# Optimization experiments

Measured on AMD Instinct MI355X. Metric: run time of the kernel, lower is better.

The kernel has to match this reference:

```python
import jax, jax.numpy as jnp
import numpy as np

H, W = 256, 256
S, S_IDX, END_BIAS = 48, 3, 10
E_IDX = S - END_BIAS          # 38
N_ITER = E_IDX - (S_IDX + 1)  # 34 sequential segments after the start segment
OUT_WIN = 10                  # outlier1d window length
OUT_THRESH = 2.0


def setup_inputs() -> dict:
    key = jax.random.key(0)
    # (x, y) event coordinates in [0, W) x [0, H); t/p/b columns are unused by the module.
    events = jax.random.uniform(key, (16, 960000, 2), jnp.float32, minval=0.0, maxval=256.0)
    return {"events": events}


def _blur(a):
    """5x5 uniform (0.04) blur, SAME padding; a: [B, S, D] -> [B, S, D]."""
    k = jnp.full((1, 1, 5, 5), 0.04, jnp.float32)
    return jax.lax.conv_general_dilated(a[:, None], k, (1, 1), [(2, 2), (2, 2)])[:, 0]


def _outlier_flags(m):
    """outlier1d(m[b, si:si+10], thresh=2)[0] for si in [S_IDX+1, E_IDX). m: [B,S] -> bool [B,N_ITER]."""
    widx = (jnp.arange(N_ITER)[:, None] + S_IDX + 1) + jnp.arange(OUT_WIN)[None, :]
    w = m[:, widx]                                   # [B, N_ITER, 10]
    med = jnp.median(w, axis=-1, keepdims=True)
    diff = jnp.abs(w - med)
    mad = jnp.median(diff, axis=-1)                  # [B, N_ITER]
    return 0.6745 * diff[..., 0] / mad > OUT_THRESH


def reference(events):
    B, N, _ = events.shape
    segmentLen = N // S            # static python int
    Nu = segmentLen * S
    x = events[:, :Nu, 0].astype(jnp.int32)   # [B, Nu]
    y = events[:, :Nu, 1].astype(jnp.int32)
    chunks = jnp.repeat(jnp.arange(S), segmentLen)   # segment id per event, [Nu]
    bidx = jnp.arange(B)[:, None]

    # per-batch x-t / y-t histograms via scatter-add
    alongX = jnp.zeros((B, S, W), jnp.float32).at[bidx, chunks[None, :], x].add(1.0)
    alongY = jnp.zeros((B, S, H), jnp.float32).at[bidx, chunks[None, :], y].add(1.0)

    def proc_axis(along, D):
        flat = along.reshape(B, -1)
        cv = (flat.mean(-1) + 3.0 * jnp.std(flat, axis=-1, ddof=1))[:, None, None]
        a = _blur(jnp.clip(along, 0.0, cv))
        m = jnp.einsum('bsd,d->bs', a, jnp.arange(D, dtype=jnp.float32)) / segmentLen
        start = m[:, S_IDX:S_IDX + 1]
        aligned = jnp.round(m - start - (D // 2 - start)).astype(jnp.int32)
        return m, aligned

    meanX, alignedX = proc_axis(alongX, W)
    meanY, alignedY = proc_axis(alongY, H)
    is_out = _outlier_flags(meanX) | _outlier_flags(meanY)   # [B, N_ITER]

    def per_batch(xb, yb, aX, aY, outb):
        xs = jnp.clip(xb - aX[chunks], 0, W - 1)
        ys = jnp.clip(yb - aY[chunks], 0, H - 1)
        idx_c = (xs + W * ys).reshape(S, segmentLen)
        idx_v = (xs // 2 + (W // 2) * (ys // 2)).reshape(S, segmentLen)
        container0 = jnp.zeros(W * H, jnp.int32).at[idx_c[S_IDX]].add(1)
        ver0 = jnp.zeros((W // 2) * (H // 2), bool).at[idx_v[S_IDX]].set(True)

        def step(carry, inp):
            container, ver, stopped = carry
            ic, iv, is_o = inp
            ver_new = ver.at[iv].set(True)
            cnt = jnp.sum(ver_new).astype(jnp.float32)
            new_info = jnp.sum(jnp.logical_xor(ver_new, ver)).astype(jnp.float32)
            brk = new_info / cnt < 0.1
            do = (~stopped) & (~is_o) & (~brk)
            stopped = stopped | ((~stopped) & (~is_o) & brk)
            container = jnp.where(do, container.at[ic].add(1), container)
            ver = jnp.where(do, ver_new, ver)
            return (container, ver, stopped), None

        (container, _, _), _ = jax.lax.scan(
            step, (container0, ver0, jnp.array(False)),
            (idx_c[S_IDX + 1:E_IDX], idx_v[S_IDX + 1:E_IDX], outb))
        c = container.astype(jnp.float32)
        cv = c.mean() + 3.0 * jnp.std(c, ddof=1)
        return jnp.clip(c, 0.0, cv) / cv

    containers = jax.vmap(per_batch)(x, y, alignedX, alignedY, is_out)  # [B, W*H]
    return containers.reshape(B, 1, H, W)
```

## Files before the change

### kernel.cpp

```cpp
#include <hip/hip_runtime.h>

#define NB 16
#define NEV 960000
#define NS 48
#define SEG 20000
#define S_IDX 3
#define E_IDX 38
#define N_ITER 34
#define ND 256
#define NCH 35

__global__ __launch_bounds__(256) void hist_kernel(const float* __restrict__ events,
                                                   float* __restrict__ alongX,
                                                   float* __restrict__ alongY,
                                                   unsigned* __restrict__ compact,
                                                   unsigned* __restrict__ container,
                                                   unsigned* __restrict__ masks,
                                                   unsigned long long* __restrict__ sums,
                                                   unsigned long long* __restrict__ cvsums) {
    __shared__ unsigned hx[4][ND], hy[4][ND];
    __shared__ unsigned long long qredX[4], qredY[4];
    int tid = threadIdx.x;
    int blk = blockIdx.x;
    int b = blk / NS, c = blk % NS;
    int wave = tid >> 6, lane = tid & 63;
    #pragma unroll
    for (int j = 0; j < 4; j++) { hx[j][tid] = 0; hy[j][tid] = 0; }
    {
        uint4 z = {0u, 0u, 0u, 0u};
        for (int i = blk * 256 + tid; i < 262144; i += NB * NS * 256)
            ((uint4*)container)[i] = z;
        for (int i = blk * 256 + tid; i < 71680; i += NB * NS * 256)
            ((uint4*)masks)[i] = z;
        if (blk == 0 && tid < NB * 2) sums[tid] = 0ull;
        if (blk == 1 && tid < NB * 2) cvsums[tid] = 0ull;
    }
    __syncthreads();
    size_t base = (size_t)b * NEV + (size_t)c * SEG;
    const float4* ev4 = (const float4*)(events + base * 2);
    bool wr = (c >= S_IDX && c < E_IDX);
    uint4* dst = wr ? (uint4*)(compact + ((size_t)b * NCH + (c - S_IDX)) * (SEG / 2)) : nullptr;
    unsigned* HX = hx[wave];
    unsigned* HY = hy[wave];
    for (int k = tid; k < SEG / 8; k += 256) {
        float4 v0 = ev4[4 * k], v1 = ev4[4 * k + 1], v2 = ev4[4 * k + 2], v3 = ev4[4 * k + 3];
        int x0 = (int)v0.x, y0 = (int)v0.y, x1 = (int)v0.z, y1 = (int)v0.w;
        int x2 = (int)v1.x, y2 = (int)v1.y, x3 = (int)v1.z, y3 = (int)v1.w;
        int x4 = (int)v2.x, y4 = (int)v2.y, x5 = (int)v2.z, y5 = (int)v2.w;
        int x6 = (int)v3.x, y6 = (int)v3.y, x7 = (int)v3.z, y7 = (int)v3.w;
        x0 = x0 > 255 ? 255 : x0; y0 = y0 > 255 ? 255 : y0;
        x1 = x1 > 255 ? 255 : x1; y1 = y1 > 255 ? 255 : y1;
        x2 = x2 > 255 ? 255 : x2; y2 = y2 > 255 ? 255 : y2;
        x3 = x3 > 255 ? 255 : x3; y3 = y3 > 255 ? 255 : y3;
        x4 = x4 > 255 ? 255 : x4; y4 = y4 > 255 ? 255 : y4;
        x5 = x5 > 255 ? 255 : x5; y5 = y5 > 255 ? 255 : y5;
        x6 = x6 > 255 ? 255 : x6; y6 = y6 > 255 ? 255 : y6;
        x7 = x7 > 255 ? 255 : x7; y7 = y7 > 255 ? 255 : y7;
        atomicAdd(&HX[x0], 1u); atomicAdd(&HY[y0], 1u);
        atomicAdd(&HX[x1], 1u); atomicAdd(&HY[y1], 1u);
        atomicAdd(&HX[x2], 1u); atomicAdd(&HY[y2], 1u);
        atomicAdd(&HX[x3], 1u); atomicAdd(&HY[y3], 1u);
        atomicAdd(&HX[x4], 1u); atomicAdd(&HY[y4], 1u);
        atomicAdd(&HX[x5], 1u); atomicAdd(&HY[y5], 1u);
        atomicAdd(&HX[x6], 1u); atomicAdd(&HY[y6], 1u);
        atomicAdd(&HX[x7], 1u); atomicAdd(&HY[y7], 1u);
        if (wr) {
            uint4 p;
            p.x = (unsigned)(x0 | (y0 << 8)) | ((unsigned)(x1 | (y1 << 8)) << 16);
            p.y = (unsigned)(x2 | (y2 << 8)) | ((unsigned)(x3 | (y3 << 8)) << 16);
            p.z = (unsigned)(x4 | (y4 << 8)) | ((unsigned)(x5 | (y5 << 8)) << 16);
            p.w = (unsigned)(x6 | (y6 << 8)) | ((unsigned)(x7 | (y7 << 8)) << 16);
            dst[k] = p;
        }
    }
    __syncthreads();
    unsigned sx = hx[0][tid] + hx[1][tid] + hx[2][tid] + hx[3][tid];
    unsigned sy = hy[0][tid] + hy[1][tid] + hy[2][tid] + hy[3][tid];
    int o = (b * NS + c) * ND + tid;
    alongX[o] = (float)sx;
    alongY[o] = (float)sy;
    unsigned long long qx = (unsigned long long)sx * sx;
    unsigned long long qy = (unsigned long long)sy * sy;
    for (int off = 32; off; off >>= 1) { qx += __shfl_down(qx, off); qy += __shfl_down(qy, off); }
    if (lane == 0) { qredX[wave] = qx; qredY[wave] = qy; }
    __syncthreads();
    if (tid == 0) {
        atomicAdd(&cvsums[b * 2],     qredX[0] + qredX[1] + qredX[2] + qredX[3]);
        atomicAdd(&cvsums[b * 2 + 1], qredY[0] + qredY[1] + qredY[2] + qredY[3]);
    }
}

__global__ __launch_bounds__(256) void stats_kernel(const float* __restrict__ alongX,
                                                    const float* __restrict__ alongY,
                                                    const unsigned long long* __restrict__ cvsums,
                                                    int* __restrict__ alignedX,
                                                    int* __restrict__ alignedY,
                                                    float* __restrict__ m_all) {
    __shared__ float sbuf[16 * ND];
    int tid = threadIdx.x;
    int blk = blockIdx.x;
    int g = blk & 3, axis = (blk >> 2) & 1, b = blk >> 3;
    const float* along = (axis ? alongY : alongX) + (size_t)b * NS * ND;
    int rbase = g * 12 - 2;
    for (int j = 0; j < 16; j++) {
        int r = rbase + j;
        if (r >= 0 && r < NS) sbuf[j * ND + tid] = along[r * ND + tid];
    }
    double ts  = 960000.0;
    double ts2 = (double)cvsums[b * 2 + axis];
    const double N = (double)(NS * ND);
    double mean = ts / N;
    double var  = (ts2 - ts * ts / N) / (N - 1.0);
    float cv = (float)(mean + 3.0 * sqrt(var));
    __syncthreads();
    int wave = tid >> 6, lane = tid & 63;
    for (int q = 0; q < 3; ++q) {
        int sI = g * 12 + wave * 3 + q;
        double acc = 0.0;
        #pragma unroll
        for (int k = 0; k < 4; ++k) {
            int d = lane + 64 * k;
            int lo = d - 2 < 0 ? 0 : d - 2;
            int hi = d + 2 > 255 ? 255 : d + 2;
            double Wd = 0.5 * (double)(lo + hi) * (double)(hi - lo + 1);
            double t = 0.0;
            #pragma unroll
            for (int ds = -2; ds <= 2; ++ds) {
                int ss = sI + ds;
                if (ss >= 0 && ss < NS) t += (double)fminf(sbuf[(ss - rbase) * ND + d], cv);
            }
            acc += t * Wd;
        }
        for (int off = 32; off; off >>= 1) acc += __shfl_down(acc, off);
        if (lane == 0) {
            float mf = (float)(acc * 0.04 / (double)SEG);
            m_all[(b * 2 + axis) * NS + sI] = mf;
            (axis ? alignedY : alignedX)[b * NS + sI] = (int)rintf(mf - 128.0f);
        }
    }
}

__global__ __launch_bounds__(256) void mask_kernel(const unsigned* __restrict__ compact,
                                                   const int* __restrict__ alignedX,
                                                   const int* __restrict__ alignedY,
                                                   unsigned* __restrict__ masks) {
    __shared__ unsigned sm[512];
    int tid = threadIdx.x, blk = blockIdx.x;
    int hi = blk & 1;
    int tile = blk >> 1;
    int b = tile / NCH, ci = tile % NCH, si = S_IDX + ci;
    sm[tid] = 0; sm[tid + 256] = 0;
    __syncthreads();
    int aX = alignedX[b * NS + si], aY = alignedY[b * NS + si];
    const uint4* cp = (const uint4*)(compact + ((size_t)b * NCH + ci) * (SEG / 2));
    for (int i = hi * 1250 + tid; i < (hi + 1) * 1250; i += 256) {
        uint4 w = cp[i];
        unsigned wsv[4] = {w.x, w.y, w.z, w.w};
        #pragma unroll
        for (int j = 0; j < 4; j++) {
            unsigned v = wsv[j];
            #pragma unroll
            for (int h = 0; h < 2; h++) {
                unsigned e = (h ? (v >> 16) : v) & 0xFFFFu;
                int xs = (int)(e & 255u) - aX; xs = xs < 0 ? 0 : (xs > 255 ? 255 : xs);
                int ys = (int)(e >> 8)   - aY; ys = ys < 0 ? 0 : (ys > 255 ? 255 : ys);
                int iv = (xs >> 1) | ((ys >> 1) << 7);
                atomicOr(&sm[iv >> 5], 1u << (iv & 31));
            }
        }
    }
    __syncthreads();
    unsigned* mo = masks + (size_t)tile * 512;
    unsigned v0 = sm[tid], v1 = sm[tid + 256];
    if (v0) atomicOr(&mo[tid], v0);
    if (v1) atomicOr(&mo[tid + 256], v1);
}

__device__ inline float median10(const float* v) {
    float w[10];
    #pragma unroll
    for (int i = 0; i < 10; i++) w[i] = v[i];
    #pragma unroll
    for (int i = 1; i < 10; i++) {
        float k = w[i]; int j = i - 1;
        while (j >= 0 && w[j] > k) { w[j + 1] = w[j]; j--; }
        w[j + 1] = k;
    }
    return 0.5f * (w[4] + w[5]);
}

__device__ inline bool outlier_flag(const float* w) {
    float med = median10(w);
    float d[10];
    #pragma unroll
    for (int i = 0; i < 10; i++) d[i] = fabsf(w[i] - med);
    float d0 = d[0];
    float mad = median10(d);
    return (0.6745f * d0 / mad) > 2.0f;
}

__device__ inline unsigned wave_sum_u32(unsigned v) {
    for (int off = 32; off; off >>= 1) v += __shfl_xor(v, off);
    return v;
}

__global__ __launch_bounds__(64) void decide_kernel(const unsigned* __restrict__ masks,
                                                    const float* __restrict__ m_all,
                                                    unsigned long long* __restrict__ commitmask) {
    int b = blockIdx.x, lane = threadIdx.x;
    const unsigned* mb = masks + (size_t)b * NCH * 512;
    uint4 v0 = ((const uint4*)mb)[lane * 2];
    uint4 v1 = ((const uint4*)mb)[lane * 2 + 1];
    const uint4* pp = (const uint4*)(mb + 512);
    uint4 p0 = pp[lane * 2], p1 = pp[lane * 2 + 1];
    bool f = false;
    if (lane < N_ITER) {
        const float* mx = m_all + b * 2 * NS;
        const float* my = mx + NS;
        f = outlier_flag(&mx[S_IDX + 1 + lane]) || outlier_flag(&my[S_IDX + 1 + lane]);
    }
    unsigned long long omask = __ballot(f);
    unsigned ver[8] = {v0.x, v0.y, v0.z, v0.w, v1.x, v1.y, v1.z, v1.w};
    unsigned pc = 0;
    #pragma unroll
    for (int j = 0; j < 8; j++) pc += __popc(ver[j]);
    unsigned cnt = wave_sum_u32(pc);
    unsigned long long cm = 1ull;
    for (int idx = 1; idx < NCH; ++idx) {
        uint4 c0 = p0, c1 = p1;
        if (idx + 1 < NCH) {
            const uint4* np = (const uint4*)(mb + (size_t)(idx + 1) * 512);
            p0 = np[lane * 2]; p1 = np[lane * 2 + 1];
        }
        unsigned del[8] = {c0.x, c0.y, c0.z, c0.w, c1.x, c1.y, c1.z, c1.w};
        unsigned nl = 0;
        #pragma unroll
        for (int j = 0; j < 8; j++) nl += __popc(del[j] & ~ver[j]);
        unsigned ni = wave_sum_u32(nl);
        bool is_o = (omask >> (idx - 1)) & 1;
        if (!is_o) {
            unsigned cn = cnt + ni;
            float ratio = (float)ni / (float)cn;
            if (ratio < 0.1f) break;
            cm |= 1ull << idx;
            cnt = cn;
            #pragma unroll
            for (int j = 0; j < 8; j++) ver[j] |= del[j];
        }
    }
    if (lane == 0) commitmask[b] = cm;
}

__global__ __launch_bounds__(256) void commit_kernel(const unsigned* __restrict__ compact,
                                                     const int* __restrict__ alignedX,
                                                     const int* __restrict__ alignedY,
                                                     const unsigned long long* __restrict__ commitmask,
                                                     unsigned* __restrict__ container) {
    int blk = blockIdx.x, tid = threadIdx.x;
    int qi = blk & 3;
    int tile = blk >> 2;
    int b = tile / NCH, ci = tile % NCH;
    if (!((commitmask[b] >> ci) & 1ull)) return;
    int si = S_IDX + ci;
    int aX = alignedX[b * NS + si], aY = alignedY[b * NS + si];
    unsigned* cont = container + (size_t)b * 65536;
    const uint4* cp = (const uint4*)(compact + ((size_t)b * NCH + ci) * (SEG / 2));
    for (int i = qi * 625 + tid; i < (qi + 1) * 625; i += 256) {
        uint4 w = cp[i];
        unsigned wsv[4] = {w.x, w.y, w.z, w.w};
        #pragma unroll
        for (int j = 0; j < 4; j++) {
            unsigned v = wsv[j];
            #pragma unroll
            for (int h = 0; h < 2; h++) {
                unsigned e = (h ? (v >> 16) : v) & 0xFFFFu;
                int xs = (int)(e & 255u) - aX; xs = xs < 0 ? 0 : (xs > 255 ? 255 : xs);
                int ys = (int)(e >> 8)   - aY; ys = ys < 0 ? 0 : (ys > 255 ? 255 : ys);
                atomicAdd(&cont[xs | (ys << 8)], 1u);
            }
        }
    }
}

__global__ __launch_bounds__(256) void cv_kernel(const unsigned* __restrict__ container,
                                                 unsigned long long* __restrict__ sums) {
    __shared__ unsigned long long sredA[4], sredB[4];
    int tid = threadIdx.x, blk = blockIdx.x;
    int b = blk >> 4, part = blk & 15;
    const uint4* c4 = (const uint4*)(container + (size_t)b * 65536) + part * 1024;
    unsigned long long s = 0, s2 = 0;
    for (int i = tid; i < 1024; i += 256) {
        uint4 v = c4[i];
        s  += (unsigned long long)v.x + v.y + v.z + v.w;
        s2 += (unsigned long long)v.x * v.x + (unsigned long long)v.y * v.y
            + (unsigned long long)v.z * v.z + (unsigned long long)v.w * v.w;
    }
    for (int off = 32; off; off >>= 1) { s += __shfl_down(s, off); s2 += __shfl_down(s2, off); }
    if ((tid & 63) == 0) { sredA[tid >> 6] = s; sredB[tid >> 6] = s2; }
    __syncthreads();
    if (tid == 0) {
        atomicAdd(&sums[b * 2],     sredA[0] + sredA[1] + sredA[2] + sredA[3]);
        atomicAdd(&sums[b * 2 + 1], sredB[0] + sredB[1] + sredB[2] + sredB[3]);
    }
}

__global__ __launch_bounds__(256) void finish_kernel(const unsigned* __restrict__ container,
                                                     const unsigned long long* __restrict__ sums,
                                                     float* __restrict__ out) {
    int g = blockIdx.x * 256 + threadIdx.x;
    int b = g >> 14;
    double ts  = (double)sums[b * 2];
    double ts2 = (double)sums[b * 2 + 1];
    double mean = ts / 65536.0;
    double var  = (ts2 - ts * ts / 65536.0) / 65535.0;
    float cv = (float)(mean + 3.0 * sqrt(var));
    uint4 v = ((const uint4*)container)[g];
    float4 o;
    o.x = fminf((float)v.x, cv) / cv;
    o.y = fminf((float)v.y, cv) / cv;
    o.z = fminf((float)v.z, cv) / cv;
    o.w = fminf((float)v.w, cv) / cv;
    ((float4*)out)[g] = o;
}

extern "C" void kernel_launch(void* const* d_in, const int* in_sizes, int n_in,
                              void* d_out, int out_size, void* d_ws, size_t ws_size,
                              hipStream_t stream) {
    const float* events = (const float*)d_in[0];
    float* out = (float*)d_out;
    char* ws = (char*)d_ws;

    float*    alongX    = (float*)(ws);
    float*    alongY    = (float*)(ws + 786432);
    unsigned* container = (unsigned*)(ws + 1572864);
    int*      alignedX  = (int*)(ws + 5767168);
    int*      alignedY  = (int*)(ws + 5770240);
    float*    m_all     = (float*)(ws + 5773312);
    unsigned long long* commitmask = (unsigned long long*)(ws + 5779456);
    unsigned long long* sums       = (unsigned long long*)(ws + 5779584);
    unsigned long long* cvsums     = (unsigned long long*)(ws + 5779840);
    unsigned* compact   = (unsigned*)(ws + 6291456);
    unsigned* masks     = (unsigned*)(ws + 29360128);

    hist_kernel<<<NB * NS, 256, 0, stream>>>(events, alongX, alongY, compact,
                                             container, masks, sums, cvsums);
    stats_kernel<<<NB * 2 * 4, 256, 0, stream>>>(alongX, alongY, cvsums,
                                                 alignedX, alignedY, m_all);
    mask_kernel<<<NB * NCH * 2, 256, 0, stream>>>(compact, alignedX, alignedY, masks);
    decide_kernel<<<NB, 64, 0, stream>>>(masks, m_all, commitmask);
    commit_kernel<<<NB * NCH * 4, 256, 0, stream>>>(compact, alignedX, alignedY,
                                                    commitmask, container);
    cv_kernel<<<NB * 16, 256, 0, stream>>>(container, sums);
    finish_kernel<<<1024, 256, 0, stream>>>(container, sums, out);
}
```

Measured before the change: 269.6 us.

## Fuse post-histogram kernels into one cooperative mega-kernel with grid syncs

```diff
diff --git a/kernel.cpp b/kernel.cpp
--- a/kernel.cpp
+++ b/kernel.cpp
@@ -1,4 +1,7 @@
 #include <hip/hip_runtime.h>
+#include <hip/hip_cooperative_groups.h>
+
+namespace cg = cooperative_groups;
 
 #define NB 16
 #define NEV 960000
@@ -9,6 +12,7 @@
 #define N_ITER 34
 #define ND 256
 #define NCH 35
+#define GRID_M 1024
 
 __global__ __launch_bounds__(256) void hist_kernel(const float* __restrict__ events,
                                                    float* __restrict__ alongX,
@@ -90,6 +94,243 @@
     }
 }
 
+__device__ inline float median10(const float* v) {
+    float w[10];
+    #pragma unroll
+    for (int i = 0; i < 10; i++) w[i] = v[i];
+    #pragma unroll
+    for (int i = 1; i < 10; i++) {
+        float k = w[i]; int j = i - 1;
+        while (j >= 0 && w[j] > k) { w[j + 1] = w[j]; j--; }
+        w[j + 1] = k;
+    }
+    return 0.5f * (w[4] + w[5]);
+}
+
+__device__ inline bool outlier_flag(const float* w) {
+    float med = median10(w);
+    float d[10];
+    #pragma unroll
+    for (int i = 0; i < 10; i++) d[i] = fabsf(w[i] - med);
+    float d0 = d[0];
+    float mad = median10(d);
+    return (0.6745f * d0 / mad) > 2.0f;
+}
+
+__device__ inline unsigned wave_sum_u32(unsigned v) {
+    for (int off = 32; off; off >>= 1) v += __shfl_xor(v, off);
+    return v;
+}
+
+__global__ __launch_bounds__(256, 4)
+void mega_kernel(const float* __restrict__ alongX,
+                 const float* __restrict__ alongY,
+                 const unsigned long long* __restrict__ cvsums,
+                 int* __restrict__ alignedX,
+                 int* __restrict__ alignedY,
+                 float* __restrict__ m_all,
+                 const unsigned* __restrict__ compact,
+                 unsigned* __restrict__ masks,
+                 unsigned long long* __restrict__ commitmask,
+                 unsigned* __restrict__ container,
+                 unsigned long long* __restrict__ sums,
+                 float* __restrict__ out) {
+    cg::grid_group grid = cg::this_grid();
+    __shared__ char smem_raw[16384] __attribute__((aligned(16)));
+    __shared__ unsigned long long credA[4], credB[4];
+    int tid = threadIdx.x, blk = blockIdx.x;
+
+    if (blk < NB * 2 * 4) {
+        float* sbuf = (float*)smem_raw;
+        int g = blk & 3, axis = (blk >> 2) & 1, b = blk >> 3;
+        const float* along = (axis ? alongY : alongX) + (size_t)b * NS * ND;
+        int rbase = g * 12 - 2;
+        for (int j = 0; j < 16; j++) {
+            int r = rbase + j;
+            if (r >= 0 && r < NS) sbuf[j * ND + tid] = along[r * ND + tid];
+        }
+        double ts  = 960000.0;
+        double ts2 = (double)cvsums[b * 2 + axis];
+        const double N = (double)(NS * ND);
+        double mean = ts / N;
+        double var  = (ts2 - ts * ts / N) / (N - 1.0);
+        float cv = (float)(mean + 3.0 * sqrt(var));
+        __syncthreads();
+        int wave = tid >> 6, lane = tid & 63;
+        for (int q = 0; q < 3; ++q) {
+            int sI = g * 12 + wave * 3 + q;
+            double acc = 0.0;
+            #pragma unroll
+            for (int k = 0; k < 4; ++k) {
+                int d = lane + 64 * k;
+                int lo = d - 2 < 0 ? 0 : d - 2;
+                int hi = d + 2 > 255 ? 255 : d + 2;
+                double Wd = 0.5 * (double)(lo + hi) * (double)(hi - lo + 1);
+                double t = 0.0;
+                #pragma unroll
+                for (int ds = -2; ds <= 2; ++ds) {
+                    int ss = sI + ds;
+                    if (ss >= 0 && ss < NS) t += (double)fminf(sbuf[(ss - rbase) * ND + d], cv);
+                }
+                acc += t * Wd;
+            }
+            for (int off = 32; off; off >>= 1) acc += __shfl_down(acc, off);
+            if (lane == 0) {
+                float mf = (float)(acc * 0.04 / (double)SEG);
+                m_all[(b * 2 + axis) * NS + sI] = mf;
+                (axis ? alignedY : alignedX)[b * NS + sI] = (int)rintf(mf - 128.0f);
+            }
+        }
+    }
+    grid.sync();
+
+    {
+        unsigned* sm = (unsigned*)smem_raw;
+        for (int t = blk; t < NB * NCH * 2; t += GRID_M) {
+            __syncthreads();
+            sm[tid] = 0; sm[tid + 256] = 0;
+            __syncthreads();
+            int hf = t & 1;
+            int tile = t >> 1;
+            int b = tile / NCH, ci = tile % NCH, si = S_IDX + ci;
+            int aX = alignedX[b * NS + si], aY = alignedY[b * NS + si];
+            const uint4* cp = (const uint4*)(compact + ((size_t)b * NCH + ci) * (SEG / 2));
+            for (int i = hf * 1250 + tid; i < (hf + 1) * 1250; i += 256) {
+                uint4 w = cp[i];
+                unsigned wsv[4] = {w.x, w.y, w.z, w.w};
+                #pragma unroll
+                for (int j = 0; j < 4; j++) {
+                    unsigned v = wsv[j];
+                    #pragma unroll
+                    for (int h = 0; h < 2; h++) {
+                        unsigned e = (h ? (v >> 16) : v) & 0xFFFFu;
+                        int xs = (int)(e & 255u) - aX; xs = xs < 0 ? 0 : (xs > 255 ? 255 : xs);
+                        int ys = (int)(e >> 8)   - aY; ys = ys < 0 ? 0 : (ys > 255 ? 255 : ys);
+                        int iv = (xs >> 1) | ((ys >> 1) << 7);
+                        atomicOr(&sm[iv >> 5], 1u << (iv & 31));
+                    }
+                }
+            }
+            __syncthreads();
+            unsigned* mo = masks + (size_t)tile * 512;
+            unsigned v0 = sm[tid], v1 = sm[tid + 256];
+            if (v0) atomicOr(&mo[tid], v0);
+            if (v1) atomicOr(&mo[tid + 256], v1);
+        }
+    }
+    grid.sync();
+
+    if (blk < NB && tid < 64) {
+        int b = blk, lane = tid;
+        const unsigned* mb = masks + (size_t)b * NCH * 512;
+        uint4 v0 = ((const uint4*)mb)[lane * 2];
+        uint4 v1 = ((const uint4*)mb)[lane * 2 + 1];
+        const uint4* pp = (const uint4*)(mb + 512);
+        uint4 p0 = pp[lane * 2], p1 = pp[lane * 2 + 1];
+        bool f = false;
+        if (lane < N_ITER) {
+            const float* mx = m_all + b * 2 * NS;
+            const float* my = mx + NS;
+            f = outlier_flag(&mx[S_IDX + 1 + lane]) || outlier_flag(&my[S_IDX + 1 + lane]);
+        }
+        unsigned long long omask = __ballot(f);
+        unsigned ver[8] = {v0.x, v0.y, v0.z, v0.w, v1.x, v1.y, v1.z, v1.w};
+        unsigned pc = 0;
+        #pragma unroll
+        for (int j = 0; j < 8; j++) pc += __popc(ver[j]);
+        unsigned cnt = wave_sum_u32(pc);
+        unsigned long long cm = 1ull;
+        for (int idx = 1; idx < NCH; ++idx) {
+            uint4 c0 = p0, c1 = p1;
+            if (idx + 1 < NCH) {
+                const uint4* np = (const uint4*)(mb + (size_t)(idx + 1) * 512);
+                p0 = np[lane * 2]; p1 = np[lane * 2 + 1];
+            }
+            unsigned del[8] = {c0.x, c0.y, c0.z, c0.w, c1.x, c1.y, c1.z, c1.w};
+            unsigned nl = 0;
+            #pragma unroll
+            for (int j = 0; j < 8; j++) nl += __popc(del[j] & ~ver[j]);
+            unsigned ni = wave_sum_u32(nl);
+            bool is_o = (omask >> (idx - 1)) & 1;
+            if (!is_o) {
+                unsigned cn = cnt + ni;
+                float ratio = (float)ni / (float)cn;
+                if (ratio < 0.1f) break;
+                cm |= 1ull << idx;
+                cnt = cn;
+                #pragma unroll
+                for (int j = 0; j < 8; j++) ver[j] |= del[j];
+            }
+        }
+        if (lane == 0) commitmask[b] = cm;
+    }
+    grid.sync();
+
+    for (int t = blk; t < NB * NCH * 4; t += GRID_M) {
+        int qi = t & 3;
+        int tile = t >> 2;
+        int b = tile / NCH, ci = tile % NCH;
+        if (!((commitmask[b] >> ci) & 1ull)) continue;
+        int si = S_IDX + ci;
+        int aX = alignedX[b * NS + si], aY = alignedY[b * NS + si];
+        unsigned* cont = container + (size_t)b * 65536;
+        const uint4* cp = (const uint4*)(compact + ((size_t)b * NCH + ci) * (SEG / 2));
+        for (int i = qi * 625 + tid; i < (qi + 1) * 625; i += 256) {
+            uint4 w = cp[i];
+            unsigned wsv[4] = {w.x, w.y, w.z, w.w};
+            #pragma unroll
+            for (int j = 0; j < 4; j++) {
+                unsigned v = wsv[j];
+                #pragma unroll
+                for (int h = 0; h < 2; h++) {
+                    unsigned e = (h ? (v >> 16) : v) & 0xFFFFu;
+                    int xs = (int)(e & 255u) - aX; xs = xs < 0 ? 0 : (xs > 255 ? 255 : xs);
+                    int ys = (int)(e >> 8)   - aY; ys = ys < 0 ? 0 : (ys > 255 ? 255 : ys);
+                    atomicAdd(&cont[xs | (ys << 8)], 1u);
+                }
+            }
+        }
+    }
+    grid.sync();
+
+    if (blk < NB * 16) {
+        int b = blk >> 4, part = blk & 15;
+        const uint4* c4 = (const uint4*)(container + (size_t)b * 65536) + part * 1024;
+        unsigned long long s = 0, s2 = 0;
+        for (int i = tid; i < 1024; i += 256) {
+            uint4 v = c4[i];
+            s  += (unsigned long long)v.x + v.y + v.z + v.w;
+            s2 += (unsigned long long)v.x * v.x + (unsigned long long)v.y * v.y
+                + (unsigned long long)v.z * v.z + (unsigned long long)v.w * v.w;
+        }
+        for (int off = 32; off; off >>= 1) { s += __shfl_down(s, off); s2 += __shfl_down(s2, off); }
+        if ((tid & 63) == 0) { credA[tid >> 6] = s; credB[tid >> 6] = s2; }
+        __syncthreads();
+        if (tid == 0) {
+            atomicAdd(&sums[b * 2],     credA[0] + credA[1] + credA[2] + credA[3]);
+            atomicAdd(&sums[b * 2 + 1], credB[0] + credB[1] + credB[2] + credB[3]);
+        }
+    }
+    grid.sync();
+
+    {
+        int g = blk * 256 + tid;
+        int b = g >> 14;
+        double ts  = (double)sums[b * 2];
+        double ts2 = (double)sums[b * 2 + 1];
+        double mean = ts / 65536.0;
+        double var  = (ts2 - ts * ts / 65536.0) / 65535.0;
+        float cv = (float)(mean + 3.0 * sqrt(var));
+        uint4 v = ((const uint4*)container)[g];
+        float4 o;
+        o.x = fminf((float)v.x, cv) / cv;
+        o.y = fminf((float)v.y, cv) / cv;
+        o.z = fminf((float)v.z, cv) / cv;
+        o.w = fminf((float)v.w, cv) / cv;
+        ((float4*)out)[g] = o;
+    }
+}
+
 __global__ __launch_bounds__(256) void stats_kernel(const float* __restrict__ alongX,
                                                     const float* __restrict__ alongY,
                                                     const unsigned long long* __restrict__ cvsums,
@@ -146,14 +387,14 @@
                                                    unsigned* __restrict__ masks) {
     __shared__ unsigned sm[512];
     int tid = threadIdx.x, blk = blockIdx.x;
-    int hi = blk & 1;
+    int hf = blk & 1;
     int tile = blk >> 1;
     int b = tile / NCH, ci = tile % NCH, si = S_IDX + ci;
     sm[tid] = 0; sm[tid + 256] = 0;
     __syncthreads();
     int aX = alignedX[b * NS + si], aY = alignedY[b * NS + si];
     const uint4* cp = (const uint4*)(compact + ((size_t)b * NCH + ci) * (SEG / 2));
-    for (int i = hi * 1250 + tid; i < (hi + 1) * 1250; i += 256) {
+    for (int i = hf * 1250 + tid; i < (hf + 1) * 1250; i += 256) {
         uint4 w = cp[i];
         unsigned wsv[4] = {w.x, w.y, w.z, w.w};
         #pragma unroll
@@ -174,34 +415,6 @@
     unsigned v0 = sm[tid], v1 = sm[tid + 256];
     if (v0) atomicOr(&mo[tid], v0);
     if (v1) atomicOr(&mo[tid + 256], v1);
-}
-
-__device__ inline float median10(const float* v) {
-    float w[10];
-    #pragma unroll
-    for (int i = 0; i < 10; i++) w[i] = v[i];
-    #pragma unroll
-    for (int i = 1; i < 10; i++) {
-        float k = w[i]; int j = i - 1;
-        while (j >= 0 && w[j] > k) { w[j + 1] = w[j]; j--; }
-        w[j + 1] = k;
-    }
-    return 0.5f * (w[4] + w[5]);
-}
-
-__device__ inline bool outlier_flag(const float* w) {
-    float med = median10(w);
-    float d[10];
-    #pragma unroll
-    for (int i = 0; i < 10; i++) d[i] = fabsf(w[i] - med);
-    float d0 = d[0];
-    float mad = median10(d);
-    return (0.6745f * d0 / mad) > 2.0f;
-}
-
-__device__ inline unsigned wave_sum_u32(unsigned v) {
-    for (int off = 32; off; off >>= 1) v += __shfl_xor(v, off);
-    return v;
 }
 
 __global__ __launch_bounds__(64) void decide_kernel(const unsigned* __restrict__ masks,
@@ -344,12 +557,27 @@
 
     hist_kernel<<<NB * NS, 256, 0, stream>>>(events, alongX, alongY, compact,
                                              container, masks, sums, cvsums);
-    stats_kernel<<<NB * 2 * 4, 256, 0, stream>>>(alongX, alongY, cvsums,
-                                                 alignedX, alignedY, m_all);
-    mask_kernel<<<NB * NCH * 2, 256, 0, stream>>>(compact, alignedX, alignedY, masks);
-    decide_kernel<<<NB, 64, 0, stream>>>(masks, m_all, commitmask);
-    commit_kernel<<<NB * NCH * 4, 256, 0, stream>>>(compact, alignedX, alignedY,
-                                                    commitmask, container);
-    cv_kernel<<<NB * 16, 256, 0, stream>>>(container, sums);
-    finish_kernel<<<1024, 256, 0, stream>>>(container, sums, out);
-}
+
+    int maxBlocksPerCU = 0;
+    hipError_t occ_err = hipOccupancyMaxActiveBlocksPerMultiprocessor(
+        &maxBlocksPerCU, (const void*)mega_kernel, 256, 0);
+    bool coop_ok = (occ_err == hipSuccess) && ((long)maxBlocksPerCU * 256 >= GRID_M);
+
+    if (coop_ok) {
+        void* args[] = {(void*)&alongX, (void*)&alongY, (void*)&cvsums,
+                        (void*)&alignedX, (void*)&alignedY, (void*)&m_all,
+                        (void*)&compact, (void*)&masks, (void*)&commitmask,
+                        (void*)&container, (void*)&sums, (void*)&out};
+        hipLaunchCooperativeKernel((const void*)mega_kernel, dim3(GRID_M), dim3(256),
+                                   args, 0, stream);
+    } else {
+        stats_kernel<<<NB * 2 * 4, 256, 0, stream>>>(alongX, alongY, cvsums,
+                                                     alignedX, alignedY, m_all);
+        mask_kernel<<<NB * NCH * 2, 256, 0, stream>>>(compact, alignedX, alignedY, masks);
+        decide_kernel<<<NB, 64, 0, stream>>>(masks, m_all, commitmask);
+        commit_kernel<<<NB * NCH * 4, 256, 0, stream>>>(compact, alignedX, alignedY,
+                                                        commitmask, container);
+        cv_kernel<<<NB * 16, 256, 0, stream>>>(container, sums);
+        finish_kernel<<<1024, 256, 0, stream>>>(container, sums, out);
+    }
+}
```

Measured after the change: 805.2 us. 2.99x slower.

## Fold stats into consumer kernels and fuse cv and finish via atomic counter

Applied to the files above, without the earlier changes.

```diff
diff --git a/kernel.cpp b/kernel.cpp
--- a/kernel.cpp
+++ b/kernel.cpp
@@ -17,7 +17,8 @@
                                                    unsigned* __restrict__ container,
                                                    unsigned* __restrict__ masks,
                                                    unsigned long long* __restrict__ sums,
-                                                   unsigned long long* __restrict__ cvsums) {
+                                                   unsigned long long* __restrict__ cvsums,
+                                                   unsigned* __restrict__ done) {
     __shared__ unsigned hx[4][ND], hy[4][ND];
     __shared__ unsigned long long qredX[4], qredY[4];
     int tid = threadIdx.x;
@@ -34,6 +35,7 @@
             ((uint4*)masks)[i] = z;
         if (blk == 0 && tid < NB * 2) sums[tid] = 0ull;
         if (blk == 1 && tid < NB * 2) cvsums[tid] = 0ull;
+        if (blk == 2 && tid == 0) *done = 0u;
     }
     __syncthreads();
     size_t base = (size_t)b * NEV + (size_t)c * SEG;
@@ -90,70 +92,60 @@
     }
 }
 
-__global__ __launch_bounds__(256) void stats_kernel(const float* __restrict__ alongX,
-                                                    const float* __restrict__ alongY,
-                                                    const unsigned long long* __restrict__ cvsums,
-                                                    int* __restrict__ alignedX,
-                                                    int* __restrict__ alignedY,
-                                                    float* __restrict__ m_all) {
-    __shared__ float sbuf[16 * ND];
-    int tid = threadIdx.x;
-    int blk = blockIdx.x;
-    int g = blk & 3, axis = (blk >> 2) & 1, b = blk >> 3;
-    const float* along = (axis ? alongY : alongX) + (size_t)b * NS * ND;
-    int rbase = g * 12 - 2;
-    for (int j = 0; j < 16; j++) {
-        int r = rbase + j;
-        if (r >= 0 && r < NS) sbuf[j * ND + tid] = along[r * ND + tid];
-    }
+__device__ inline float centroid_m(const float* __restrict__ along, float cv,
+                                   int si, int lane) {
+    double acc = 0.0;
+    #pragma unroll
+    for (int k = 0; k < 4; ++k) {
+        int d = lane + 64 * k;
+        int lo = d - 2 < 0 ? 0 : d - 2;
+        int hi = d + 2 > 255 ? 255 : d + 2;
+        double Wd = 0.5 * (double)(lo + hi) * (double)(hi - lo + 1);
+        double t = 0.0;
+        #pragma unroll
+        for (int ds = -2; ds <= 2; ++ds) {
+            int ss = si + ds;
+            if (ss >= 0 && ss < NS) t += (double)fminf(along[ss * ND + d], cv);
+        }
+        acc += t * Wd;
+    }
+    for (int off = 32; off; off >>= 1) acc += __shfl_down(acc, off);
+    return (float)(acc * 0.04 / (double)SEG);
+}
+
+__device__ inline float axis_cv(const unsigned long long* __restrict__ cvsums,
+                                int b, int axis) {
     double ts  = 960000.0;
     double ts2 = (double)cvsums[b * 2 + axis];
     const double N = (double)(NS * ND);
     double mean = ts / N;
     double var  = (ts2 - ts * ts / N) / (N - 1.0);
-    float cv = (float)(mean + 3.0 * sqrt(var));
-    __syncthreads();
-    int wave = tid >> 6, lane = tid & 63;
-    for (int q = 0; q < 3; ++q) {
-        int sI = g * 12 + wave * 3 + q;
-        double acc = 0.0;
-        #pragma unroll
-        for (int k = 0; k < 4; ++k) {
-            int d = lane + 64 * k;
-            int lo = d - 2 < 0 ? 0 : d - 2;
-            int hi = d + 2 > 255 ? 255 : d + 2;
-            double Wd = 0.5 * (double)(lo + hi) * (double)(hi - lo + 1);
-            double t = 0.0;
-            #pragma unroll
-            for (int ds = -2; ds <= 2; ++ds) {
-                int ss = sI + ds;
-                if (ss >= 0 && ss < NS) t += (double)fminf(sbuf[(ss - rbase) * ND + d], cv);
-            }
-            acc += t * Wd;
-        }
-        for (int off = 32; off; off >>= 1) acc += __shfl_down(acc, off);
-        if (lane == 0) {
-            float mf = (float)(acc * 0.04 / (double)SEG);
-            m_all[(b * 2 + axis) * NS + sI] = mf;
-            (axis ? alignedY : alignedX)[b * NS + sI] = (int)rintf(mf - 128.0f);
-        }
-    }
+    return (float)(mean + 3.0 * sqrt(var));
 }
 
 __global__ __launch_bounds__(256) void mask_kernel(const unsigned* __restrict__ compact,
-                                                   const int* __restrict__ alignedX,
-                                                   const int* __restrict__ alignedY,
+                                                   const float* __restrict__ alongX,
+                                                   const float* __restrict__ alongY,
+                                                   const unsigned long long* __restrict__ cvsums,
                                                    unsigned* __restrict__ masks) {
     __shared__ unsigned sm[512];
+    __shared__ int s_al[2];
     int tid = threadIdx.x, blk = blockIdx.x;
-    int hi = blk & 1;
+    int hf = blk & 1;
     int tile = blk >> 1;
     int b = tile / NCH, ci = tile % NCH, si = S_IDX + ci;
     sm[tid] = 0; sm[tid + 256] = 0;
-    __syncthreads();
-    int aX = alignedX[b * NS + si], aY = alignedY[b * NS + si];
+    int wave = tid >> 6, lane = tid & 63;
+    if (wave < 2) {
+        const float* along = (wave ? alongY : alongX) + (size_t)b * NS * ND;
+        float cv = axis_cv(cvsums, b, wave);
+        float mf = centroid_m(along, cv, si, lane);
+        if (lane == 0) s_al[wave] = (int)rintf(mf - 128.0f);
+    }
+    __syncthreads();
+    int aX = s_al[0], aY = s_al[1];
     const uint4* cp = (const uint4*)(compact + ((size_t)b * NCH + ci) * (SEG / 2));
-    for (int i = hi * 1250 + tid; i < (hi + 1) * 1250; i += 256) {
+    for (int i = hf * 1250 + tid; i < (hf + 1) * 1250; i += 256) {
         uint4 w = cp[i];
         unsigned wsv[4] = {w.x, w.y, w.z, w.w};
         #pragma unroll
@@ -204,65 +196,89 @@
     return v;
 }
 
-__global__ __launch_bounds__(64) void decide_kernel(const unsigned* __restrict__ masks,
-                                                    const float* __restrict__ m_all,
-                                                    unsigned long long* __restrict__ commitmask) {
-    int b = blockIdx.x, lane = threadIdx.x;
-    const unsigned* mb = masks + (size_t)b * NCH * 512;
-    uint4 v0 = ((const uint4*)mb)[lane * 2];
-    uint4 v1 = ((const uint4*)mb)[lane * 2 + 1];
-    const uint4* pp = (const uint4*)(mb + 512);
-    uint4 p0 = pp[lane * 2], p1 = pp[lane * 2 + 1];
-    bool f = false;
-    if (lane < N_ITER) {
-        const float* mx = m_all + b * 2 * NS;
-        const float* my = mx + NS;
-        f = outlier_flag(&mx[S_IDX + 1 + lane]) || outlier_flag(&my[S_IDX + 1 + lane]);
-    }
-    unsigned long long omask = __ballot(f);
-    unsigned ver[8] = {v0.x, v0.y, v0.z, v0.w, v1.x, v1.y, v1.z, v1.w};
-    unsigned pc = 0;
-    #pragma unroll
-    for (int j = 0; j < 8; j++) pc += __popc(ver[j]);
-    unsigned cnt = wave_sum_u32(pc);
-    unsigned long long cm = 1ull;
-    for (int idx = 1; idx < NCH; ++idx) {
-        uint4 c0 = p0, c1 = p1;
-        if (idx + 1 < NCH) {
-            const uint4* np = (const uint4*)(mb + (size_t)(idx + 1) * 512);
-            p0 = np[lane * 2]; p1 = np[lane * 2 + 1];
-        }
-        unsigned del[8] = {c0.x, c0.y, c0.z, c0.w, c1.x, c1.y, c1.z, c1.w};
-        unsigned nl = 0;
+__global__ __launch_bounds__(256) void decide_kernel(const unsigned* __restrict__ masks,
+                                                     const float* __restrict__ alongX,
+                                                     const float* __restrict__ alongY,
+                                                     const unsigned long long* __restrict__ cvsums,
+                                                     unsigned long long* __restrict__ commitmask) {
+    __shared__ float m_s[2][NS];
+    int tid = threadIdx.x, b = blockIdx.x;
+    int wave = tid >> 6, lane = tid & 63;
+    float cv0 = axis_cv(cvsums, b, 0);
+    float cv1 = axis_cv(cvsums, b, 1);
+    const float* alX = alongX + (size_t)b * NS * ND;
+    const float* alY = alongY + (size_t)b * NS * ND;
+    for (int t = wave; t < 86; t += 4) {
+        int axis = t & 1, si = 4 + (t >> 1);
+        const float* along = axis ? alY : alX;
+        float mf = centroid_m(along, axis ? cv1 : cv0, si, lane);
+        if (lane == 0) m_s[axis][si] = mf;
+    }
+    __syncthreads();
+    if (tid < 64) {
+        bool f = false;
+        if (tid < N_ITER)
+            f = outlier_flag(&m_s[0][S_IDX + 1 + tid]) || outlier_flag(&m_s[1][S_IDX + 1 + tid]);
+        unsigned long long omask = __ballot(f);
+        const unsigned* mb = masks + (size_t)b * NCH * 512;
+        uint4 v0 = ((const uint4*)mb)[lane * 2];
+        uint4 v1 = ((const uint4*)mb)[lane * 2 + 1];
+        const uint4* pp = (const uint4*)(mb + 512);
+        uint4 p0 = pp[lane * 2], p1 = pp[lane * 2 + 1];
+        unsigned ver[8] = {v0.x, v0.y, v0.z, v0.w, v1.x, v1.y, v1.z, v1.w};
+        unsigned pc = 0;
         #pragma unroll
-        for (int j = 0; j < 8; j++) nl += __popc(del[j] & ~ver[j]);
-        unsigned ni = wave_sum_u32(nl);
-        bool is_o = (omask >> (idx - 1)) & 1;
-        if (!is_o) {
-            unsigned cn = cnt + ni;
-            float ratio = (float)ni / (float)cn;
-            if (ratio < 0.1f) break;
-            cm |= 1ull << idx;
-            cnt = cn;
+        for (int j = 0; j < 8; j++) pc += __popc(ver[j]);
+        unsigned cnt = wave_sum_u32(pc);
+        unsigned long long cm = 1ull;
+        for (int idx = 1; idx < NCH; ++idx) {
+            uint4 c0 = p0, c1 = p1;
+            if (idx + 1 < NCH) {
+                const uint4* np = (const uint4*)(mb + (size_t)(idx + 1) * 512);
+                p0 = np[lane * 2]; p1 = np[lane * 2 + 1];
+            }
+            unsigned del[8] = {c0.x, c0.y, c0.z, c0.w, c1.x, c1.y, c1.z, c1.w};
+            unsigned nl = 0;
             #pragma unroll
-            for (int j = 0; j < 8; j++) ver[j] |= del[j];
-        }
-    }
-    if (lane == 0) commitmask[b] = cm;
+            for (int j = 0; j < 8; j++) nl += __popc(del[j] & ~ver[j]);
+            unsigned ni = wave_sum_u32(nl);
+            bool is_o = (omask >> (idx - 1)) & 1;
+            if (!is_o) {
+                unsigned cn = cnt + ni;
+                float ratio = (float)ni / (float)cn;
+                if (ratio < 0.1f) break;
+                cm |= 1ull << idx;
+                cnt = cn;
+                #pragma unroll
+                for (int j = 0; j < 8; j++) ver[j] |= del[j];
+            }
+        }
+        if (lane == 0) commitmask[b] = cm;
+    }
 }
 
 __global__ __launch_bounds__(256) void commit_kernel(const unsigned* __restrict__ compact,
-                                                     const int* __restrict__ alignedX,
-                                                     const int* __restrict__ alignedY,
+                                                     const float* __restrict__ alongX,
+                                                     const float* __restrict__ alongY,
+                                                     const unsigned long long* __restrict__ cvsums,
                                                      const unsigned long long* __restrict__ commitmask,
                                                      unsigned* __restrict__ container) {
+    __shared__ int s_al[2];
     int blk = blockIdx.x, tid = threadIdx.x;
     int qi = blk & 3;
     int tile = blk >> 2;
     int b = tile / NCH, ci = tile % NCH;
     if (!((commitmask[b] >> ci) & 1ull)) return;
     int si = S_IDX + ci;
-    int aX = alignedX[b * NS + si], aY = alignedY[b * NS + si];
+    int wave = tid >> 6, lane = tid & 63;
+    if (wave < 2) {
+        const float* along = (wave ? alongY : alongX) + (size_t)b * NS * ND;
+        float cv = axis_cv(cvsums, b, wave);
+        float mf = centroid_m(along, cv, si, lane);
+        if (lane == 0) s_al[wave] = (int)rintf(mf - 128.0f);
+    }
+    __syncthreads();
+    int aX = s_al[0], aY = s_al[1];
     unsigned* cont = container + (size_t)b * 65536;
     const uint4* cp = (const uint4*)(compact + ((size_t)b * NCH + ci) * (SEG / 2));
     for (int i = qi * 625 + tid; i < (qi + 1) * 625; i += 256) {
@@ -282,38 +298,52 @@
     }
 }
 
-__global__ __launch_bounds__(256) void cv_kernel(const unsigned* __restrict__ container,
-                                                 unsigned long long* __restrict__ sums) {
+__global__ __launch_bounds__(256) void cvfinish_kernel(const unsigned* __restrict__ container,
+                                                       unsigned long long* __restrict__ sums,
+                                                       unsigned* __restrict__ done,
+                                                       float* __restrict__ out) {
     __shared__ unsigned long long sredA[4], sredB[4];
+    __shared__ float s_cv[NB];
     int tid = threadIdx.x, blk = blockIdx.x;
-    int b = blk >> 4, part = blk & 15;
-    const uint4* c4 = (const uint4*)(container + (size_t)b * 65536) + part * 1024;
-    unsigned long long s = 0, s2 = 0;
-    for (int i = tid; i < 1024; i += 256) {
-        uint4 v = c4[i];
-        s  += (unsigned long long)v.x + v.y + v.z + v.w;
-        s2 += (unsigned long long)v.x * v.x + (unsigned long long)v.y * v.y
-            + (unsigned long long)v.z * v.z + (unsigned long long)v.w * v.w;
-    }
-    for (int off = 32; off; off >>= 1) { s += __shfl_down(s, off); s2 += __shfl_down(s2, off); }
-    if ((tid & 63) == 0) { sredA[tid >> 6] = s; sredB[tid >> 6] = s2; }
-    __syncthreads();
+    if (blk < 256) {
+        int b = blk >> 4, part = blk & 15;
+        const uint4* c4 = (const uint4*)(container + (size_t)b * 65536) + part * 1024;
+        unsigned long long s = 0, s2 = 0;
+        for (int i = tid; i < 1024; i += 256) {
+            uint4 v = c4[i];
+            s  += (unsigned long long)v.x + v.y + v.z + v.w;
+            s2 += (unsigned long long)v.x * v.x + (unsigned long long)v.y * v.y
+                + (unsigned long long)v.z * v.z + (unsigned long long)v.w * v.w;
+        }
+        for (int off = 32; off; off >>= 1) { s += __shfl_down(s, off); s2 += __shfl_down(s2, off); }
+        if ((tid & 63) == 0) { sredA[tid >> 6] = s; sredB[tid >> 6] = s2; }
+        __syncthreads();
+        if (tid == 0) {
+            atomicAdd(&sums[b * 2],     sredA[0] + sredA[1] + sredA[2] + sredA[3]);
+            atomicAdd(&sums[b * 2 + 1], sredB[0] + sredB[1] + sredB[2] + sredB[3]);
+            __threadfence();
+            atomicAdd(done, 1u);
+        }
+    }
     if (tid == 0) {
-        atomicAdd(&sums[b * 2],     sredA[0] + sredA[1] + sredA[2] + sredA[3]);
-        atomicAdd(&sums[b * 2 + 1], sredB[0] + sredB[1] + sredB[2] + sredB[3]);
-    }
-}
-
-__global__ __launch_bounds__(256) void finish_kernel(const unsigned* __restrict__ container,
-                                                     const unsigned long long* __restrict__ sums,
-                                                     float* __restrict__ out) {
-    int g = blockIdx.x * 256 + threadIdx.x;
+        while (__hip_atomic_load(done, __ATOMIC_ACQUIRE, __HIP_MEMORY_SCOPE_AGENT) < 256u)
+            __builtin_amdgcn_s_sleep(32);
+        for (int b = 0; b < NB; b++) {
+            unsigned long long ts_u  = __hip_atomic_load(&sums[b * 2],
+                                         __ATOMIC_RELAXED, __HIP_MEMORY_SCOPE_AGENT);
+            unsigned long long ts2_u = __hip_atomic_load(&sums[b * 2 + 1],
+                                         __ATOMIC_RELAXED, __HIP_MEMORY_SCOPE_AGENT);
+            double ts  = (double)ts_u;
+            double ts2 = (double)ts2_u;
+            double mean = ts / 65536.0;
+            double var  = (ts2 - ts * ts / 65536.0) / 65535.0;
+            s_cv[b] = (float)(mean + 3.0 * sqrt(var));
+        }
+    }
+    __syncthreads();
+    int g = blk * 256 + tid;
     int b = g >> 14;
-    double ts  = (double)sums[b * 2];
-    double ts2 = (double)sums[b * 2 + 1];
-    double mean = ts / 65536.0;
-    double var  = (ts2 - ts * ts / 65536.0) / 65535.0;
-    float cv = (float)(mean + 3.0 * sqrt(var));
+    float cv = s_cv[b];
     uint4 v = ((const uint4*)container)[g];
     float4 o;
     o.x = fminf((float)v.x, cv) / cv;
@@ -333,23 +363,18 @@
     float*    alongX    = (float*)(ws);
     float*    alongY    = (float*)(ws + 786432);
     unsigned* container = (unsigned*)(ws + 1572864);
-    int*      alignedX  = (int*)(ws + 5767168);
-    int*      alignedY  = (int*)(ws + 5770240);
-    float*    m_all     = (float*)(ws + 5773312);
     unsigned long long* commitmask = (unsigned long long*)(ws + 5779456);
     unsigned long long* sums       = (unsigned long long*)(ws + 5779584);
     unsigned long long* cvsums     = (unsigned long long*)(ws + 5779840);
+    unsigned* done      = (unsigned*)(ws + 5780096);
     unsigned* compact   = (unsigned*)(ws + 6291456);
     unsigned* masks     = (unsigned*)(ws + 29360128);
 
     hist_kernel<<<NB * NS, 256, 0, stream>>>(events, alongX, alongY, compact,
-                                             container, masks, sums, cvsums);
-    stats_kernel<<<NB * 2 * 4, 256, 0, stream>>>(alongX, alongY, cvsums,
-                                                 alignedX, alignedY, m_all);
-    mask_kernel<<<NB * NCH * 2, 256, 0, stream>>>(compact, alignedX, alignedY, masks);
-    decide_kernel<<<NB, 64, 0, stream>>>(masks, m_all, commitmask);
-    commit_kernel<<<NB * NCH * 4, 256, 0, stream>>>(compact, alignedX, alignedY,
+                                             container, masks, sums, cvsums, done);
+    mask_kernel<<<NB * NCH * 2, 256, 0, stream>>>(compact, alongX, alongY, cvsums, masks);
+    decide_kernel<<<NB, 256, 0, stream>>>(masks, alongX, alongY, cvsums, commitmask);
+    commit_kernel<<<NB * NCH * 4, 256, 0, stream>>>(compact, alongX, alongY, cvsums,
                                                     commitmask, container);
-    cv_kernel<<<NB * 16, 256, 0, stream>>>(container, sums);
-    finish_kernel<<<1024, 256, 0, stream>>>(container, sums, out);
-}
+    cvfinish_kernel<<<1024, 256, 0, stream>>>(container, sums, done, out);
+}
```

Result: slower. 371.2 us (+37.7%).
